# Kernel tuning notes

Measured on AMD Instinct MI355X. Metric: run time of the kernel, lower is better.

## Reference

```python
import jax, jax.numpy as jnp
import numpy as np

B, C, IMG, P = 8, 3, 64, 8
E, H, BS, L, NC = 256, 2, 8, 128, 10
HD = E // H
N = (IMG // P) ** 2 + 1  # 65 tokens (64 patches + cls)
NEG = -1e30  # stands in for -inf fill of block-diagonal scores
SCALE = float(np.sqrt(HD))


def _ln(x, g, b):
    m = jnp.mean(x, -1, keepdims=True)
    v = jnp.mean((x - m) ** 2, -1, keepdims=True)
    return (x - m) * jax.lax.rsqrt(v + 1e-5) * g + b


def _sparse_attn(x, wq, bq, wk, bk, wv, bv, fp):
    # Block-diagonal attention: only bs x bs diagonal blocks are finite, so we
    # reshape into non-overlapping blocks instead of materializing (B,N,H,N).
    Bx, Nx, Ex = x.shape
    q = (x @ wq + bq).reshape(Bx, Nx, H, HD)
    k = (x @ wk + bk).reshape(Bx, Nx, H, HD)
    v = (x @ wv + bv).reshape(Bx, Nx, H, HD)
    q = jnp.einsum('bnhe,ei->bnhi', q, fp)
    k = jnp.einsum('bnhe,ei->bnhi', k, fp)
    pad = (-Nx) % BS
    Np = Nx + pad
    G = Np // BS
    padf = lambda t: jnp.pad(t, ((0, 0), (0, pad), (0, 0), (0, 0)))
    qb = padf(q).reshape(Bx, G, BS, H, HD)
    kb = padf(k).reshape(Bx, G, BS, H, HD)
    vb = padf(v).reshape(Bx, G, BS, H, HD)
    scores = jnp.einsum('bgqhd,bgkhd->bgqhk', qb, kb) / SCALE  # (B,G,bs,H,bs)
    valid = (jnp.arange(Np) < Nx).reshape(G, BS)  # mask padded keys in last block
    scores = jnp.where(valid[None, :, None, None, :], scores, NEG)
    attn = jax.nn.softmax(scores, axis=-1)
    out = jnp.einsum('bgqhk,bgkhd->bgqhd', attn, vb).reshape(Bx, Np, Ex)
    return out[:, :Nx]


def setup_inputs() -> dict:
    key = jax.random.key(0)
    ks = jax.random.split(key, 12)
    s = 0.02
    f = lambda k, shp: (jax.random.normal(k, shp, jnp.float32) * s)
    z = lambda shp: jnp.zeros(shp, jnp.float32)
    o = lambda shp: jnp.ones(shp, jnp.float32)
    return {
        'src': jax.random.normal(ks[0], (B, C, IMG, IMG), jnp.float32),
        'conv_w': f(ks[1], (E, C, P, P)),
        'conv_b': z((E,)),
        'pos_emb': f(ks[2], (1, N, E)),
        'cls_tok': z((1, 1, E)),
        'Wq': f(ks[3], (L, E, E)), 'bq': z((L, E)),
        'Wk': f(ks[4], (L, E, E)), 'bk': z((L, E)),
        'Wv': f(ks[5], (L, E, E)), 'bv': z((L, E)),
        'fproj': f(ks[6], (L, HD, HD)),
        'ln1_g': o((L, E)), 'ln1_b': z((L, E)),
        'ln2_g': o((L, E)), 'ln2_b': z((L, E)),
        'ff1_w': f(ks[7], (L, E, 4 * E)), 'ff1_b': z((L, 4 * E)),
        'ff2_w': f(ks[8], (L, 4 * E, E)), 'ff2_b': z((L, E)),
        'fc_w': f(ks[9], (E, NC)), 'fc_b': z((NC,)),
    }


def reference(src, conv_w, conv_b, pos_emb, cls_tok, Wq, bq, Wk, bk, Wv, bv,
              fproj, ln1_g, ln1_b, ln2_g, ln2_b, ff1_w, ff1_b, ff2_w, ff2_b,
              fc_w, fc_b):
    # patch embedding (Conv2d stride=patch) -> flatten(2).transpose(1,2)
    x = jax.lax.conv_general_dilated(
        src, conv_w, (P, P), 'VALID',
        dimension_numbers=('NCHW', 'OIHW', 'NCHW')) + conv_b[None, :, None, None]
    x = x.reshape(B, E, -1).transpose(0, 2, 1)  # (B, num_patches, E)
    x = jnp.concatenate([jnp.broadcast_to(cls_tok, (B, 1, E)), x], axis=1)
    x = x + pos_emb

    params = (Wq, bq, Wk, bk, Wv, bv, fproj, ln1_g, ln1_b, ln2_g, ln2_b,
              ff1_w, ff1_b, ff2_w, ff2_b)

    def enc(h, p):
        wq, bq_, wk, bk_, wv, bv_, fp, g1, b1, g2, b2, w1, bb1, w2, bb2 = p
        h = h + _sparse_attn(_ln(h, g1, b1), wq, bq_, wk, bk_, wv, bv_, fp)
        hn = _ln(h, g2, b2)
        hf = jax.nn.gelu(hn @ w1 + bb1, approximate=False)  # dropout = eval identity
        h = h + hf @ w2 + bb2
        return h, None

    x, _ = jax.lax.scan(enc, x, params)
    return x[:, 0] @ fc_w + fc_b
```

## Files before the change

### kernel.cpp

```cpp
#include <hip/hip_runtime.h>
#include <math.h>

typedef __attribute__((ext_vector_type(8))) short short8v;
typedef __attribute__((ext_vector_type(4))) float float4v;

#if defined(__has_builtin)
#if __has_builtin(__builtin_amdgcn_global_load_lds)
#define USE_GLL 1
#endif
#endif
#ifndef USE_GLL
#define USE_GLL 0
#endif

__device__ __forceinline__ float gelu_f(float v) {
    return 0.5f * v * (1.0f + erff(v * 0.70710678118654752440f));
}

__device__ __forceinline__ unsigned short bf16r(float f) {
    unsigned u = __float_as_uint(f);
    u += 0x7FFFu + ((u >> 16) & 1u);
    return (unsigned short)(u >> 16);
}

__device__ __forceinline__ float bf2f(unsigned short s) {
    return __uint_as_float(((unsigned)s) << 16);
}

__global__ void dump_k(float* __restrict__ out, int n, float val) {
    int t = blockIdx.x * 256 + threadIdx.x;
    if (t < n) out[t] = val;
}

__global__ void tc_k(const float* __restrict__ in0, unsigned short* __restrict__ out0,
                     int R, int Cc, long long ils, long long ols) {
    __shared__ float tile[32][33];
    int l = blockIdx.z;
    const float* in = in0 + (size_t)l * ils;
    unsigned short* out = out0 + (size_t)l * ols;
    int t = threadIdx.x;
    int tx = t & 31, ty = t >> 5;
    int r0 = blockIdx.x * 32, c0 = blockIdx.y * 32;
#pragma unroll
    for (int i = 0; i < 4; ++i) {
        int r = r0 + ty + i * 8, c = c0 + tx;
        tile[ty + i * 8][tx] = (r < R && c < Cc) ? in[(size_t)r * Cc + c] : 0.f;
    }
    __syncthreads();
#pragma unroll
    for (int i = 0; i < 4; ++i) {
        int c = c0 + ty + i * 8, r = r0 + tx;
        if (c < Cc && r < R) out[(size_t)c * R + r] = bf16r(tile[tx][ty + i * 8]);
    }
}

__global__ void fold_k(const float* __restrict__ Wq0, const float* __restrict__ Wk0,
                       const float* __restrict__ fp0, unsigned short* __restrict__ Wt0,
                       int E, int HD, int mode) {
    extern __shared__ float fpS[];
    int l = blockIdx.z;
    long long EE = (long long)E * E;
    const float* fp = fp0 + (size_t)l * HD * HD;
    unsigned short* Wt = Wt0 + (size_t)l * 3 * EE;
    int t = threadIdx.x;
    int n0 = blockIdx.x * 64;
    int n = n0 + (t & 63);
    int cg = t >> 6;

    int i0 = 0;
    if (mode == 0) {
        for (int idx = t; idx < HD * HD; idx += 256) fpS[idx] = fp[idx];
    } else if (mode == 1) {
        int base = (n0 < E) ? n0 : n0 - E;
        i0 = base % HD;
        for (int idx = t; idx < HD * 64; idx += 256)
            fpS[idx] = fp[(size_t)(idx >> 6) * HD + i0 + (idx & 63)];
    }
    __syncthreads();
    if (n >= 2 * E) return;
    int s = (n >= E) ? 1 : 0;
    int idd = n - s * E;
    int h = idd / HD, i = idd % HD;
    const float* W = (s ? Wk0 : Wq0) + (size_t)l * EE;
    for (int c = cg; c < E; c += 4) {
        const float* Wr = W + (size_t)c * E + h * HD;
        float acc = 0.f;
        if (mode == 0) {
            for (int d = 0; d < HD; ++d) acc += Wr[d] * fpS[d * HD + i];
        } else if (mode == 1) {
            for (int d = 0; d < HD; ++d) acc += Wr[d] * fpS[d * 64 + (i - i0)];
        } else {
            for (int d = 0; d < HD; ++d) acc += Wr[d] * fp[(size_t)d * HD + i];
        }
        Wt[(size_t)n * E + c] = bf16r(acc);
    }
}

__global__ void biasfold_k(const float* __restrict__ bq0, const float* __restrict__ bk0,
                           const float* __restrict__ bv0, const float* __restrict__ fp0,
                           float* __restrict__ bqkv0, int E, int HD) {
    int l = blockIdx.z;
    const float* bq = bq0 + (size_t)l * E;
    const float* bk = bk0 + (size_t)l * E;
    const float* bv = bv0 + (size_t)l * E;
    const float* fp = fp0 + (size_t)l * HD * HD;
    float* bqkv = bqkv0 + (size_t)l * 3 * E;
    int c = blockIdx.x * 256 + threadIdx.x;
    if (c >= 3 * E) return;
    if (c < 2 * E) {
        int mat = c / E, cc = c % E, h = cc / HD, j = cc % HD;
        const float* bb = mat ? bk : bq;
        float s = 0.f;
        for (int d = 0; d < HD; ++d) s += bb[h * HD + d] * fp[(size_t)d * HD + j];
        bqkv[c] = s;
    } else {
        bqkv[c] = bv[c - 2 * E];
    }
}

__global__ __launch_bounds__(512) void gemm2_k(
        const unsigned short* __restrict__ A, int lda,
        const unsigned short* __restrict__ Bt, int ldbt,
        void* __restrict__ Cv, int ldc,
        const float* __restrict__ bias,
        int M, int Nn, int K, int op, int al, int nNt) {
    __shared__ unsigned short Ab[128 * 64];
    __shared__ unsigned short Bb[128 * 64];
    int t = threadIdx.x;
    int nwg = gridDim.x;
    int orig = blockIdx.x;
    int xcd = orig & 7, pos = orig >> 3;
    int q = nwg >> 3, r = nwg & 7;
    int wgid = (xcd < r ? xcd * (q + 1) : r * (q + 1) + (xcd - r) * q) + pos;
    int m0 = (wgid / nNt) * 128, n0 = (wgid % nNt) * 128;
    int w = t >> 6, lane = t & 63;
    int wm = w >> 2, wn = w & 3;
    int lrow = lane & 15, lk = lane >> 4;

    float4v acc[4][2];
#pragma unroll
    for (int fa = 0; fa < 4; ++fa)
#pragma unroll
        for (int fb = 0; fb < 2; ++fb) acc[fa][fb] = (float4v){0.f, 0.f, 0.f, 0.f};

    int srow8 = lane >> 3;
    int sch = lane & 7;
    bool fastA = al && (m0 + 128 <= M);
    bool fastB = al && (n0 + 128 <= Nn);

    for (int k0 = 0; k0 < K; k0 += 64) {
        bool fullK = (k0 + 64 <= K);
        __syncthreads();
#if USE_GLL
        if (fastA && fullK) {
#pragma unroll
            for (int it = 0; it < 2; ++it) {
                int rr = w * 16 + it * 8 + srow8;
                const unsigned short* g = A + (size_t)(m0 + rr) * lda + k0 + ((sch ^ (rr & 7)) << 3);
                __builtin_amdgcn_global_load_lds((const void*)g, (void*)&Ab[(w * 16 + it * 8) * 64], 16, 0, 0);
            }
        } else
#endif
        {
#pragma unroll
            for (int cc = 0; cc < 2; ++cc) {
                int c = t + cc * 512;
                int row = c >> 3, ch = c & 7;
                int gm = m0 + row, gk = k0 + ch * 8;
                short8v v = {0, 0, 0, 0, 0, 0, 0, 0};
                if (gm < M) {
                    if (al && gk + 8 <= K) {
                        v = *(const short8v*)(A + (size_t)gm * lda + gk);
                    } else {
                        const unsigned short* p = A + (size_t)gm * lda;
#pragma unroll
                        for (int j = 0; j < 8; ++j)
                            if (gk + j < K) v[j] = (short)p[gk + j];
                    }
                }
                *(short8v*)&Ab[row * 64 + ((ch ^ (row & 7)) << 3)] = v;
            }
        }
#if USE_GLL
        if (fastB && fullK) {
#pragma unroll
            for (int it = 0; it < 2; ++it) {
                int rr = w * 16 + it * 8 + srow8;
                const unsigned short* g = Bt + (size_t)(n0 + rr) * ldbt + k0 + ((sch ^ (rr & 7)) << 3);
                __builtin_amdgcn_global_load_lds((const void*)g, (void*)&Bb[(w * 16 + it * 8) * 64], 16, 0, 0);
            }
        } else
#endif
        {
#pragma unroll
            for (int cc = 0; cc < 2; ++cc) {
                int c = t + cc * 512;
                int row = c >> 3, ch = c & 7;
                int gn = n0 + row, gk = k0 + ch * 8;
                short8v v = {0, 0, 0, 0, 0, 0, 0, 0};
                if (gn < Nn) {
                    if (al && gk + 8 <= K) {
                        v = *(const short8v*)(Bt + (size_t)gn * ldbt + gk);
                    } else {
                        const unsigned short* p = Bt + (size_t)gn * ldbt;
#pragma unroll
                        for (int j = 0; j < 8; ++j)
                            if (gk + j < K) v[j] = (short)p[gk + j];
                    }
                }
                *(short8v*)&Bb[row * 64 + ((ch ^ (row & 7)) << 3)] = v;
            }
        }
        __syncthreads();
#pragma unroll
        for (int ks = 0; ks < 2; ++ks) {
            short8v af[4], bf[2];
#pragma unroll
            for (int fa = 0; fa < 4; ++fa) {
                int row = wm * 64 + fa * 16 + lrow;
                af[fa] = *(const short8v*)&Ab[row * 64 + (((ks * 4 + lk) ^ (row & 7)) << 3)];
            }
#pragma unroll
            for (int fb = 0; fb < 2; ++fb) {
                int row = wn * 32 + fb * 16 + lrow;
                bf[fb] = *(const short8v*)&Bb[row * 64 + (((ks * 4 + lk) ^ (row & 7)) << 3)];
            }
#pragma unroll
            for (int fa = 0; fa < 4; ++fa)
#pragma unroll
                for (int fb = 0; fb < 2; ++fb)
                    acc[fa][fb] = __builtin_amdgcn_mfma_f32_16x16x32_bf16(
                        af[fa], bf[fb], acc[fa][fb], 0, 0, 0);
        }
    }
    float* Cf = (float*)Cv;
    unsigned short* Cu = (unsigned short*)Cv;
#pragma unroll
    for (int fb = 0; fb < 2; ++fb) {
        int col = n0 + wn * 32 + fb * 16 + lrow;
        if (col >= Nn) continue;
        float bb = bias ? bias[col] : 0.f;
#pragma unroll
        for (int fa = 0; fa < 4; ++fa) {
#pragma unroll
            for (int q2 = 0; q2 < 4; ++q2) {
                int row = m0 + wm * 64 + fa * 16 + lk * 4 + q2;
                if (row >= M) continue;
                float v = acc[fa][fb][q2] + bb;
                size_t idx = (size_t)row * ldc + col;
                if (op == 0) Cf[idx] = v;
                else if (op == 1) Cu[idx] = bf16r(gelu_f(v));
                else if (op == 2) Cf[idx] += v;
                else Cu[idx] = bf16r(v);
            }
        }
    }
}

__global__ void embed_lds_k(const float* __restrict__ src, const float* __restrict__ cw,
                            const float* __restrict__ cb, const float* __restrict__ pos,
                            const float* __restrict__ cls, float* __restrict__ x,
                            int C, int IMG, int P, int m, int E, int N, int K) {
    extern __shared__ float patch[];
    int n = blockIdx.x, b = blockIdx.y, t = threadIdx.x;
    if (n == 0) {
        for (int e = t; e < E; e += 256)
            x[((size_t)b * N) * E + e] = cls[e] + pos[e];
        return;
    }
    int p = n - 1, ph = p / m, pw = p % m;
    int P2 = P * P;
    for (int mm = t; mm < K; mm += 256) {
        int c = mm / P2, rem = mm % P2, i = rem / P, j = rem % P;
        patch[mm] = src[(((size_t)b * C + c) * IMG + ph * P + i) * IMG + pw * P + j];
    }
    __syncthreads();
    for (int e = t; e < E; e += 256) {
        float acc = cb[e];
        const float* wr = cw + (size_t)e * K;
        for (int mm = 0; mm < K; ++mm) acc += patch[mm] * wr[mm];
        x[((size_t)b * N + n) * E + e] = acc + pos[(size_t)n * E + e];
    }
}

__global__ void embed_dir_k(const float* __restrict__ src, const float* __restrict__ cw,
                            const float* __restrict__ cb, const float* __restrict__ pos,
                            const float* __restrict__ cls, float* __restrict__ x,
                            int C, int IMG, int P, int m, int E, int N, int K) {
    int n = blockIdx.x, b = blockIdx.y, t = threadIdx.x;
    if (n == 0) {
        for (int e = t; e < E; e += 256)
            x[((size_t)b * N) * E + e] = cls[e] + pos[e];
        return;
    }
    int p = n - 1, ph = p / m, pw = p % m;
    int P2 = P * P;
    for (int e = t; e < E; e += 256) {
        float acc = cb[e];
        const float* wr = cw + (size_t)e * K;
        for (int mm = 0; mm < K; ++mm) {
            int c = mm / P2, rem = mm % P2, i = rem / P, j = rem % P;
            acc += src[(((size_t)b * C + c) * IMG + ph * P + i) * IMG + pw * P + j] * wr[mm];
        }
        x[((size_t)b * N + n) * E + e] = acc + pos[(size_t)n * E + e];
    }
}

__global__ void ln_k(const float* __restrict__ x, const float* __restrict__ g,
                     const float* __restrict__ b, unsigned short* __restrict__ xg,
                     int TOK, int E, float invE) {
    int row = blockIdx.x * 4 + (threadIdx.x >> 6);
    int lane = threadIdx.x & 63;
    if (row >= TOK) return;
    const float* xr = x + (size_t)row * E;
    float s = 0.f;
    for (int e = lane; e < E; e += 64) s += xr[e];
#pragma unroll
    for (int mm = 32; mm >= 1; mm >>= 1) s += __shfl_xor(s, mm, 64);
    float mean = s * invE;
    float v = 0.f;
    for (int e = lane; e < E; e += 64) { float d = xr[e] - mean; v += d * d; }
#pragma unroll
    for (int mm = 32; mm >= 1; mm >>= 1) v += __shfl_xor(v, mm, 64);
    float inv = rsqrtf(v * invE + 1e-5f);
    unsigned short* orow = xg + (size_t)row * E;
    for (int e = lane; e < E; e += 64)
        orow[e] = bf16r((xr[e] - mean) * inv * g[e] + b[e]);
}

__global__ void attn_sm_k(const unsigned short* __restrict__ qkv, float* __restrict__ x,
                          unsigned short* __restrict__ xg,
                          const float* __restrict__ g2, const float* __restrict__ b2,
                          int img0, int N, int E, int H, int HD, float rscale,
                          float invE, int vec) {
    extern __shared__ float sc[];
    int g = blockIdx.x, im = blockIdx.y, t = threadIdx.x;
    int t0 = g * 8, nv = min(8, N - t0);
    int E3 = 3 * E;
    const unsigned short* qb = qkv + ((size_t)im * N + t0) * E3;
    size_t rowbase = ((size_t)(img0 + im)) * N + t0;
    float* xb = x + rowbase * E;
    for (int idx = t; idx < H * 64; idx += 256) {
        int h = idx >> 6, qr = (idx >> 3) & 7, kr = idx & 7;
        float s = 0.f;
        if (qr < nv && kr < nv) {
            const unsigned short* qp = qb + (size_t)qr * E3 + h * HD;
            const unsigned short* kp = qb + (size_t)kr * E3 + E + h * HD;
            if (vec) {
                for (int d = 0; d < HD; d += 8) {
                    short8v qv = *(const short8v*)(qp + d);
                    short8v kv = *(const short8v*)(kp + d);
#pragma unroll
                    for (int j = 0; j < 8; ++j)
                        s += bf2f((unsigned short)qv[j]) * bf2f((unsigned short)kv[j]);
                }
            } else {
                for (int d = 0; d < HD; ++d)
                    s += bf2f(qp[d]) * bf2f(kp[d]);
            }
        }
        sc[idx] = s * rscale;
    }
    __syncthreads();
    for (int idx = t; idx < H * 8; idx += 256) {
        int h = idx >> 3, qr = idx & 7;
        if (qr < nv) {
            float* row = sc + h * 64 + qr * 8;
            float mx = -1e30f;
            for (int k = 0; k < nv; ++k) mx = fmaxf(mx, row[k]);
            float sum = 0.f;
            for (int k = 0; k < nv; ++k) { float e = expf(row[k] - mx); row[k] = e; sum += e; }
            float inv = 1.f / sum;
            for (int k = 0; k < nv; ++k) row[k] *= inv;
        }
    }
    __syncthreads();
    for (int c = t; c < E; c += 256) {
        int h = c / HD;
        const float* srow = sc + h * 64;
        float vcol[8];
#pragma unroll
        for (int k = 0; k < 8; ++k)
            vcol[k] = (k < nv) ? bf2f(qb[(size_t)k * E3 + 2 * E + c]) : 0.f;
        for (int r = 0; r < nv; ++r) {
            float o = 0.f;
#pragma unroll
            for (int k = 0; k < 8; ++k) o += srow[r * 8 + k] * vcol[k];
            xb[(size_t)r * E + c] += o;
        }
    }
    __syncthreads();
    int w = t >> 6, lane = t & 63;
#pragma unroll
    for (int rr = 0; rr < 2; ++rr) {
        int r = w + rr * 4;
        if (r >= nv) continue;
        const float* xr = xb + (size_t)r * E;
        float s = 0.f;
        for (int e = lane; e < E; e += 64) s += xr[e];
#pragma unroll
        for (int mm = 32; mm >= 1; mm >>= 1) s += __shfl_xor(s, mm, 64);
        float mean = s * invE;
        float v = 0.f;
        for (int e = lane; e < E; e += 64) { float d = xr[e] - mean; v += d * d; }
#pragma unroll
        for (int mm = 32; mm >= 1; mm >>= 1) v += __shfl_xor(v, mm, 64);
        float inv = rsqrtf(v * invE + 1e-5f);
        unsigned short* orow = xg + (rowbase + r) * E;
        for (int e = lane; e < E; e += 64)
            orow[e] = bf16r((xr[e] - mean) * inv * g2[e] + b2[e]);
    }
}

__global__ void head_k(const float* __restrict__ fw, const float* __restrict__ fb,
                       const float* __restrict__ x, float* __restrict__ out,
                       int Bc, int N, int E, int NC) {
    int idx = blockIdx.x * 256 + threadIdx.x;
    if (idx < Bc * NC) {
        int b = idx / NC, nc = idx % NC;
        float acc = fb[nc];
        const float* xr = x + (size_t)b * N * E;
        for (int e = 0; e < E; ++e) acc += xr[e] * fw[(size_t)e * NC + nc];
        out[idx] = acc;
    }
}

static int isqrt_i(long long v) {
    if (v < 0) return -1;
    long long r = (long long)(sqrt((double)v) + 0.5);
    while (r * r > v) --r;
    while ((r + 1) * (r + 1) <= v) ++r;
    return (int)r;
}

extern "C" void kernel_launch(void* const* d_in, const int* in_sizes, int n_in,
                              void* d_out, int out_size, void* d_ws, size_t ws_size,
                              hipStream_t stream) {
    float* out = (float*)d_out;
    int nblk_out = (out_size + 255) / 256;
#define DUMP(code, val) do { \
        dump_k<<<nblk_out, 256, 0, stream>>>(out, out_size, (float)((code) * 1000000.0 + (double)(val))); \
        return; } while (0)

    if (n_in != 22) DUMP(1, n_in < 999999 ? n_in : 999999);
    const int* S = in_sizes;

    int E = S[2];
    if (E <= 0 || S[4] != E) DUMP(2, 4);
    if (S[6] % E) DUMP(2, 6);
    int L = S[6] / E;
    if (L <= 0) DUMP(2, 6);
    long long EE = (long long)E * E;
    if (S[5] != L * EE || S[7] != L * EE || S[9] != L * EE) DUMP(2, 5);
    if (S[8] != L * E || S[10] != L * E) DUMP(2, 8);
    if (S[12] != L * E || S[13] != L * E || S[14] != L * E || S[15] != L * E) DUMP(2, 12);
    if (S[19] != L * E) DUMP(2, 19);
    if (S[11] % L) DUMP(2, 11);
    int HD = isqrt_i(S[11] / L);
    if ((long long)HD * HD * L != S[11] || HD <= 0 || E % HD) DUMP(3, HD > 0 ? HD : 0);
    int H = E / HD;
    if (S[17] % L) DUMP(2, 17);
    int FF = S[17] / L;
    if (S[16] != (long long)L * E * FF) DUMP(2, 16);
    if (S[18] != (long long)L * FF * E) DUMP(2, 18);
    if (S[3] % E) DUMP(2, 3);
    int N = S[3] / E;
    int m = isqrt_i(N - 1);
    if (m <= 0 || m * m != N - 1) DUMP(4, N < 999999 ? N : 999999);
    int NC = S[21];
    if (NC <= 0 || S[20] != (long long)E * NC) DUMP(2, 20);
    if (out_size % NC) DUMP(8, out_size < 999999 ? out_size : 999999);
    int Bc = out_size / NC;
    if (S[1] % E) DUMP(2, 1);
    int K = S[1] / E;
    static const int corder[12] = {3, 4, 1, 2, 8, 16, 6, 12, 32, 64, 24, 48};
    int C = -1, P = -1;
    for (int ci = 0; ci < 12; ++ci) {
        int c = corder[ci];
        if (K % c) continue;
        int p = isqrt_i(K / c);
        if (p > 0 && p * p * c == K) {
            long long img = (long long)p * m;
            if ((long long)Bc * c * img * img == S[0]) { C = c; P = p; break; }
        }
    }
    if (C < 0) DUMP(5, K < 999999 ? K : 999999);
    int IMG = P * m;
    int TOK = Bc * N;
    int Gg = (N + 7) / 8;
    int E3 = 3 * E;
    int al = ((E % 8) == 0 && (FF % 8) == 0) ? 1 : 0;
    int vecA = (al && (HD % 8) == 0) ? 1 : 0;

    int fmode;
    if (HD <= 64) fmode = 0;
    else if ((E % 64) == 0 && HD <= 256) fmode = 1;
    else fmode = 2;
    size_t fold_sh = (fmode == 0) ? (size_t)HD * HD * 4
                   : (fmode == 1) ? (size_t)HD * 64 * 4 : 16;

    size_t b_x  = ((size_t)TOK * E * 4 + 255) & ~(size_t)255;
    size_t b_xg = ((size_t)TOK * E * 2 + 255) & ~(size_t)255;
    size_t s_wt  = ((size_t)E3 * E * 2 + 255) & ~(size_t)255;
    size_t s_wff = ((size_t)E * FF * 2 + 255) & ~(size_t)255;
    size_t s_bq  = ((size_t)E3 * 4 + 255) & ~(size_t)255;
    size_t perL = s_wt + 2 * s_wff + s_bq;
    size_t minbuf = (size_t)N * E3 * 2;
    size_t fb2 = (size_t)128 * FF * 2;
    if (fb2 > minbuf) minbuf = fb2;

    int LW;
    if (b_x + b_xg + perL * L + minbuf <= ws_size) LW = L;
    else if (b_x + b_xg + perL + minbuf <= ws_size) LW = 1;
    else { DUMP(6, (double)(ws_size >> 20)); }

    char* wsb = (char*)d_ws;
    size_t off = 0;
    float* x = (float*)(wsb + off); off += b_x;
    unsigned short* xg = (unsigned short*)(wsb + off); off += b_xg;
    unsigned short* Wt_base = (unsigned short*)(wsb + off); off += s_wt * LW;
    unsigned short* w1t_base = (unsigned short*)(wsb + off); off += s_wff * LW;
    unsigned short* w2t_base = (unsigned short*)(wsb + off); off += s_wff * LW;
    float* bq_base = (float*)(wsb + off); off += s_bq * LW;
    size_t buf_bytes = ws_size - off;
    unsigned short* bufu = (unsigned short*)(wsb + off);

    int CHI = (int)(buf_bytes / ((size_t)N * E3 * 2));
    if (CHI > Bc) CHI = Bc;
    long long chf_l = (long long)(buf_bytes / ((size_t)FF * 2));
    chf_l = (chf_l / 128) * 128;
    int CHF = chf_l > TOK ? TOK : (int)chf_l;
    if (CHI < 1 || CHF < 128) DUMP(6, (double)(ws_size >> 20));

    const float* src = (const float*)d_in[0];
    const float* cw  = (const float*)d_in[1];
    const float* cb  = (const float*)d_in[2];
    const float* pos = (const float*)d_in[3];
    const float* cls = (const float*)d_in[4];
    const float* Wq  = (const float*)d_in[5];
    const float* bq  = (const float*)d_in[6];
    const float* Wk  = (const float*)d_in[7];
    const float* bk  = (const float*)d_in[8];
    const float* Wv  = (const float*)d_in[9];
    const float* bv  = (const float*)d_in[10];
    const float* fp  = (const float*)d_in[11];
    const float* g1  = (const float*)d_in[12];
    const float* b1  = (const float*)d_in[13];
    const float* g2  = (const float*)d_in[14];
    const float* b2  = (const float*)d_in[15];
    const float* w1  = (const float*)d_in[16];
    const float* bb1 = (const float*)d_in[17];
    const float* w2  = (const float*)d_in[18];
    const float* bb2 = (const float*)d_in[19];
    const float* fcw = (const float*)d_in[20];
    const float* fcb = (const float*)d_in[21];

    float invE = 1.f / (float)E;
    float rscale = 1.f / sqrtf((float)HD);
    size_t wtL = (size_t)E3 * E;
    size_t wffL = (size_t)E * FF;

    size_t patch_sh = (size_t)K * sizeof(float);
    if (patch_sh <= 48000)
        embed_lds_k<<<dim3(N, Bc), 256, patch_sh, stream>>>(src, cw, cb, pos, cls, x,
                                                            C, IMG, P, m, E, N, K);
    else
        embed_dir_k<<<dim3(N, Bc), 256, 0, stream>>>(src, cw, cb, pos, cls, x,
                                                     C, IMG, P, m, E, N, K);

    int gx_fold = (2 * E + 63) / 64;
    if (LW == L) {
        fold_k<<<dim3(gx_fold, 1, L), 256, fold_sh, stream>>>(Wq, Wk, fp, Wt_base, E, HD, fmode);
        tc_k<<<dim3((E + 31) / 32, (E + 31) / 32, L), 256, 0, stream>>>(
            Wv, Wt_base + (size_t)2 * E * E, E, E, EE, wtL);
        tc_k<<<dim3((E + 31) / 32, (FF + 31) / 32, L), 256, 0, stream>>>(
            w1, w1t_base, E, FF, (long long)E * FF, wffL);
        tc_k<<<dim3((FF + 31) / 32, (E + 31) / 32, L), 256, 0, stream>>>(
            w2, w2t_base, FF, E, (long long)E * FF, wffL);
        biasfold_k<<<dim3((E3 + 255) / 256, 1, L), 256, 0, stream>>>(
            bq, bk, bv, fp, bq_base, E, HD);
    }

    int ln_grid = (TOK + 3) / 4;
    size_t attn_sh = (size_t)H * 64 * sizeof(float);

    for (int l = 0; l < L; ++l) {
        int lw = (LW == L) ? l : 0;
        unsigned short* Wt_l  = Wt_base + (size_t)lw * (s_wt / 2);
        unsigned short* w1t_l = w1t_base + (size_t)lw * (s_wff / 2);
        unsigned short* w2t_l = w2t_base + (size_t)lw * (s_wff / 2);
        float* bq_l = (float*)((char*)bq_base + (size_t)lw * s_bq);

        if (LW != L) {
            fold_k<<<dim3(gx_fold, 1, 1), 256, fold_sh, stream>>>(
                Wq + (size_t)l * EE, Wk + (size_t)l * EE, fp + (size_t)l * HD * HD,
                Wt_l, E, HD, fmode);
            tc_k<<<dim3((E + 31) / 32, (E + 31) / 32, 1), 256, 0, stream>>>(
                Wv + (size_t)l * EE, Wt_l + (size_t)2 * E * E, E, E, 0, 0);
            tc_k<<<dim3((E + 31) / 32, (FF + 31) / 32, 1), 256, 0, stream>>>(
                w1 + (size_t)l * E * FF, w1t_l, E, FF, 0, 0);
            tc_k<<<dim3((FF + 31) / 32, (E + 31) / 32, 1), 256, 0, stream>>>(
                w2 + (size_t)l * FF * E, w2t_l, FF, E, 0, 0);
            biasfold_k<<<dim3((E3 + 255) / 256, 1, 1), 256, 0, stream>>>(
                bq + (size_t)l * E, bk + (size_t)l * E, bv + (size_t)l * E,
                fp + (size_t)l * HD * HD, bq_l, E, HD);
        }

        ln_k<<<ln_grid, 256, 0, stream>>>(x, g1 + (size_t)l * E, b1 + (size_t)l * E,
                                          xg, TOK, E, invE);
        for (int img0 = 0; img0 < Bc; img0 += CHI) {
            int nimg = Bc - img0 < CHI ? Bc - img0 : CHI;
            int ntok = nimg * N;
            int nMt = (ntok + 127) / 128, nNt = (E3 + 127) / 128;
            gemm2_k<<<nMt * nNt, 512, 0, stream>>>(
                xg + (size_t)img0 * N * E, E, Wt_l, E, bufu, E3, bq_l,
                ntok, E3, E, 3, al, nNt);
            attn_sm_k<<<dim3(Gg, nimg), 256, attn_sh, stream>>>(
                bufu, x, xg, g2 + (size_t)l * E, b2 + (size_t)l * E,
                img0, N, E, H, HD, rscale, invE, vecA);
        }
        for (int tok0 = 0; tok0 < TOK; tok0 += CHF) {
            int ntok = TOK - tok0 < CHF ? TOK - tok0 : CHF;
            int nMt = (ntok + 127) / 128;
            int nNt1 = (FF + 127) / 128, nNt2 = (E + 127) / 128;
            gemm2_k<<<nMt * nNt1, 512, 0, stream>>>(
                xg + (size_t)tok0 * E, E, w1t_l, E, bufu, FF,
                bb1 + (size_t)l * FF, ntok, FF, E, 1, al, nNt1);
            gemm2_k<<<nMt * nNt2, 512, 0, stream>>>(
                bufu, FF, w2t_l, FF, x + (size_t)tok0 * E, E,
                bb2 + (size_t)l * E, ntok, E, FF, 2, al, nNt2);
        }
    }
    head_k<<<nblk_out, 256, 0, stream>>>(fcw, fcb, x, out, Bc, N, E, NC);
#undef DUMP
}
```

Measured before the change: 10.15 ms.

## Add 256x256-tile pipelined bf16 MFMA GEMM with remainder fallback

Introduces a 256x256 tile GEMM kernel using direct global-to-LDS loads, XOR-swizzled LDS, double buffering, and XCD-aware block remapping, plus a launcher that splits M into a 256-aligned part and a remainder handled by the old 128-tile kernel. The FFN token chunk is rounded to multiples of 256. The intent is more data reuse per block and better overlap of loads with MFMA. At these small token counts it leaves very few blocks and adds an extra launch per GEMM.

```diff
diff --git a/kernel.cpp b/kernel.cpp
--- a/kernel.cpp
+++ b/kernel.cpp
@@ -254,6 +254,203 @@
                 else Cu[idx] = bf16r(v);
             }
         }
+    }
+}
+
+__global__ __launch_bounds__(512, 2) void gemm256_k(
+        const unsigned short* __restrict__ A, int lda,
+        const unsigned short* __restrict__ Bt, int ldbt,
+        void* __restrict__ Cv, int ldc,
+        const float* __restrict__ bias,
+        int M, int Nn, int K, int op, int nNt) {
+    extern __shared__ unsigned short lds[];
+    const int t = threadIdx.x;
+    const int w = t >> 6, lane = t & 63;
+    const int wm = w >> 2, wn = w & 3;
+    const int lrow = lane & 15, lk = lane >> 4;
+    int nwg = gridDim.x, orig = blockIdx.x;
+    int xcd = orig & 7, pos = orig >> 3;
+    int q = nwg >> 3, r = nwg & 7;
+    int wgid = (xcd < r ? xcd * (q + 1) : r * (q + 1) + (xcd - r) * q) + pos;
+    const int m0 = (wgid / nNt) * 256, n0 = (wgid % nNt) * 256;
+
+    const int sg_row = lane >> 3;
+    const int sg_ch = (lane & 7) ^ sg_row;
+
+    float4v acc[8][4];
+#pragma unroll
+    for (int fa = 0; fa < 8; ++fa)
+#pragma unroll
+        for (int fb = 0; fb < 4; ++fb) acc[fa][fb] = (float4v){0.f, 0.f, 0.f, 0.f};
+
+    const int nk = K >> 6;
+
+#if USE_GLL
+#define STAGE_A(KT, HALF, SLOT)                                                          \
+    {                                                                                    \
+        _Pragma("unroll")                                                                \
+        for (int it = 0; it < 2; ++it) {                                                 \
+            int rl = (HALF) * 128 + w * 16 + it * 8;                                     \
+            const unsigned short* g = A + (size_t)(m0 + rl + sg_row) * lda +             \
+                                      (KT) * 64 + (sg_ch << 3);                          \
+            __builtin_amdgcn_global_load_lds((const void*)g,                             \
+                (void*)&lds[(size_t)(SLOT) * 16384 + (size_t)rl * 64], 16, 0, 0);        \
+        }                                                                                \
+    }
+#define STAGE_B(KT, HALF, SLOT)                                                          \
+    {                                                                                    \
+        _Pragma("unroll")                                                                \
+        for (int it = 0; it < 2; ++it) {                                                 \
+            int rl = (HALF) * 128 + w * 16 + it * 8;                                     \
+            const unsigned short* g = Bt + (size_t)(n0 + rl + sg_row) * ldbt +           \
+                                      (KT) * 64 + (sg_ch << 3);                          \
+            __builtin_amdgcn_global_load_lds((const void*)g,                             \
+                (void*)&lds[32768 + (size_t)(SLOT) * 16384 + (size_t)rl * 64], 16, 0, 0);\
+        }                                                                                \
+    }
+#else
+#define STAGE_A(KT, HALF, SLOT)                                                          \
+    {                                                                                    \
+        _Pragma("unroll")                                                                \
+        for (int it = 0; it < 2; ++it) {                                                 \
+            int rl = (HALF) * 128 + w * 16 + it * 8;                                     \
+            const unsigned short* g = A + (size_t)(m0 + rl + sg_row) * lda +             \
+                                      (KT) * 64 + (sg_ch << 3);                          \
+            *(short8v*)&lds[(size_t)(SLOT) * 16384 + (size_t)(rl + sg_row) * 64 +        \
+                            ((size_t)((lane & 7)) << 3)] = *(const short8v*)g;           \
+        }                                                                                \
+    }
+#define STAGE_B(KT, HALF, SLOT)                                                          \
+    {                                                                                    \
+        _Pragma("unroll")                                                                \
+        for (int it = 0; it < 2; ++it) {                                                 \
+            int rl = (HALF) * 128 + w * 16 + it * 8;                                     \
+            const unsigned short* g = Bt + (size_t)(n0 + rl + sg_row) * ldbt +           \
+                                      (KT) * 64 + (sg_ch << 3);                          \
+            *(short8v*)&lds[32768 + (size_t)(SLOT) * 16384 + (size_t)(rl + sg_row) * 64 +\
+                            ((size_t)((lane & 7)) << 3)] = *(const short8v*)g;           \
+        }                                                                                \
+    }
+#endif
+
+    STAGE_A(0, 0, 0); STAGE_A(0, 1, 0); STAGE_B(0, 0, 0); STAGE_B(0, 1, 0);
+    if (nk > 1) { STAGE_B(1, 0, 1); STAGE_B(1, 1, 1); }
+    __builtin_amdgcn_sched_barrier(0);
+#if USE_GLL
+    if (nk > 1) asm volatile("s_waitcnt vmcnt(4)" ::: "memory");
+    else        asm volatile("s_waitcnt vmcnt(0)" ::: "memory");
+#else
+    asm volatile("s_waitcnt vmcnt(0)" ::: "memory");
+#endif
+    __builtin_amdgcn_sched_barrier(0);
+    __builtin_amdgcn_s_barrier();
+    __builtin_amdgcn_sched_barrier(0);
+
+    short8v breg[4][2];
+    for (int tt = 0; tt < nk; ++tt) {
+        const int s = tt & 1, sn = s ^ 1;
+        const bool doA = (tt + 1) < nk;
+        const bool doB = (tt + 2) < nk;
+        const size_t aBase = (size_t)s * 16384;
+        const size_t bBase = 32768 + (size_t)s * 16384;
+#pragma unroll
+        for (int p = 0; p < 4; ++p) {
+            short8v areg[2][2];
+            if (p == 0) {
+#pragma unroll
+                for (int fb = 0; fb < 4; ++fb) {
+                    int row = wn * 64 + fb * 16 + lrow;
+#pragma unroll
+                    for (int ks = 0; ks < 2; ++ks)
+                        breg[fb][ks] = *(const short8v*)&lds[bBase + (size_t)row * 64 +
+                            ((((ks << 2) + lk) ^ (row & 7)) << 3)];
+                }
+            }
+#pragma unroll
+            for (int i = 0; i < 2; ++i) {
+                int row = wm * 128 + (2 * p + i) * 16 + lrow;
+#pragma unroll
+                for (int ks = 0; ks < 2; ++ks)
+                    areg[i][ks] = *(const short8v*)&lds[aBase + (size_t)row * 64 +
+                        ((((ks << 2) + lk) ^ (row & 7)) << 3)];
+            }
+            if (p == 0 && doA) STAGE_A(tt + 1, 0, sn);
+            if (p == 1 && doA) STAGE_A(tt + 1, 1, sn);
+            if (p == 2 && doB) STAGE_B(tt + 2, 0, s);
+            if (p == 3 && doB) STAGE_B(tt + 2, 1, s);
+            __builtin_amdgcn_sched_barrier(0);
+            __builtin_amdgcn_s_barrier();
+            __builtin_amdgcn_sched_barrier(0);
+            __builtin_amdgcn_s_setprio(1);
+#pragma unroll
+            for (int i = 0; i < 2; ++i)
+#pragma unroll
+                for (int fb = 0; fb < 4; ++fb)
+#pragma unroll
+                    for (int ks = 0; ks < 2; ++ks)
+                        acc[2 * p + i][fb] = __builtin_amdgcn_mfma_f32_16x16x32_bf16(
+                            areg[i][ks], breg[fb][ks], acc[2 * p + i][fb], 0, 0, 0);
+            __builtin_amdgcn_s_setprio(0);
+            __builtin_amdgcn_sched_barrier(0);
+            if (p == 3) {
+#if USE_GLL
+                if (doB)      asm volatile("s_waitcnt vmcnt(4)" ::: "memory");
+                else if (doA) asm volatile("s_waitcnt vmcnt(0)" ::: "memory");
+#else
+                asm volatile("s_waitcnt vmcnt(0)" ::: "memory");
+#endif
+                __builtin_amdgcn_sched_barrier(0);
+            }
+            __builtin_amdgcn_s_barrier();
+            __builtin_amdgcn_sched_barrier(0);
+        }
+    }
+#undef STAGE_A
+#undef STAGE_B
+
+    float* Cf = (float*)Cv;
+    unsigned short* Cu = (unsigned short*)Cv;
+#pragma unroll
+    for (int fb = 0; fb < 4; ++fb) {
+        int col = n0 + wn * 64 + fb * 16 + lrow;
+        float bb = bias ? bias[col] : 0.f;
+#pragma unroll
+        for (int fa = 0; fa < 8; ++fa) {
+#pragma unroll
+            for (int q2 = 0; q2 < 4; ++q2) {
+                int row = m0 + wm * 128 + fa * 16 + lk * 4 + q2;
+                float v = acc[fa][fb][q2] + bb;
+                size_t idx = (size_t)row * ldc + col;
+                if (op == 0) Cf[idx] = v;
+                else if (op == 1) Cu[idx] = bf16r(gelu_f(v));
+                else if (op == 2) Cf[idx] += v;
+                else Cu[idx] = bf16r(v);
+            }
+        }
+    }
+}
+
+static inline void launch_gemm(const unsigned short* A, int lda,
+                               const unsigned short* Bt, int ldbt,
+                               void* Cv, int ldc, const float* bias,
+                               int M, int Nn, int K, int op, int al,
+                               hipStream_t stream) {
+    int M256 = 0;
+    if (al && Nn % 256 == 0 && K % 128 == 0 && K >= 128) M256 = (M / 256) * 256;
+    if (M256 > 0) {
+        int nNt = Nn / 256;
+        int grid = (M256 / 256) * nNt;
+        gemm256_k<<<grid, 512, 131072, stream>>>(A, lda, Bt, ldbt, Cv, ldc, bias,
+                                                 M256, Nn, K, op, nNt);
+    }
+    int Mr = M - M256;
+    if (Mr > 0) {
+        int esz = (op == 0 || op == 2) ? 4 : 2;
+        int nNt = (Nn + 127) / 128;
+        int grid = ((Mr + 127) / 128) * nNt;
+        gemm2_k<<<grid, 512, 0, stream>>>(A + (size_t)M256 * lda, lda, Bt, ldbt,
+                                          (void*)((char*)Cv + (size_t)M256 * ldc * esz),
+                                          ldc, bias, Mr, Nn, K, op, al, nNt);
     }
 }
 
@@ -492,6 +689,9 @@
     int al = ((E % 8) == 0 && (FF % 8) == 0) ? 1 : 0;
     int vecA = (al && (HD % 8) == 0) ? 1 : 0;
 
+    (void)hipFuncSetAttribute((const void*)gemm256_k,
+                              hipFuncAttributeMaxDynamicSharedMemorySize, 131072);
+
     int fmode;
     if (HD <= 64) fmode = 0;
     else if ((E % 64) == 0 && HD <= 256) fmode = 1;
@@ -528,7 +728,7 @@
     int CHI = (int)(buf_bytes / ((size_t)N * E3 * 2));
     if (CHI > Bc) CHI = Bc;
     long long chf_l = (long long)(buf_bytes / ((size_t)FF * 2));
-    chf_l = (chf_l / 128) * 128;
+    chf_l = (chf_l / 256) * 256;
     int CHF = chf_l > TOK ? TOK : (int)chf_l;
     if (CHI < 1 || CHF < 128) DUMP(6, (double)(ws_size >> 20));
 
@@ -611,24 +811,18 @@
         for (int img0 = 0; img0 < Bc; img0 += CHI) {
             int nimg = Bc - img0 < CHI ? Bc - img0 : CHI;
             int ntok = nimg * N;
-            int nMt = (ntok + 127) / 128, nNt = (E3 + 127) / 128;
-            gemm2_k<<<nMt * nNt, 512, 0, stream>>>(
-                xg + (size_t)img0 * N * E, E, Wt_l, E, bufu, E3, bq_l,
-                ntok, E3, E, 3, al, nNt);
+            launch_gemm(xg + (size_t)img0 * N * E, E, Wt_l, E, bufu, E3, bq_l,
+                        ntok, E3, E, 3, al, stream);
             attn_sm_k<<<dim3(Gg, nimg), 256, attn_sh, stream>>>(
                 bufu, x, xg, g2 + (size_t)l * E, b2 + (size_t)l * E,
                 img0, N, E, H, HD, rscale, invE, vecA);
         }
         for (int tok0 = 0; tok0 < TOK; tok0 += CHF) {
             int ntok = TOK - tok0 < CHF ? TOK - tok0 : CHF;
-            int nMt = (ntok + 127) / 128;
-            int nNt1 = (FF + 127) / 128, nNt2 = (E + 127) / 128;
-            gemm2_k<<<nMt * nNt1, 512, 0, stream>>>(
-                xg + (size_t)tok0 * E, E, w1t_l, E, bufu, FF,
-                bb1 + (size_t)l * FF, ntok, FF, E, 1, al, nNt1);
-            gemm2_k<<<nMt * nNt2, 512, 0, stream>>>(
-                bufu, FF, w2t_l, FF, x + (size_t)tok0 * E, E,
-                bb2 + (size_t)l * E, ntok, E, FF, 2, al, nNt2);
+            launch_gemm(xg + (size_t)tok0 * E, E, w1t_l, E, bufu, FF,
+                        bb1 + (size_t)l * FF, ntok, FF, E, 1, al, stream);
+            launch_gemm(bufu, FF, w2t_l, FF, x + (size_t)tok0 * E, E,
+                        bb2 + (size_t)l * E, ntok, E, FF, 2, al, stream);
         }
     }
     head_k<<<nblk_out, 256, 0, stream>>>(fcw, fcb, x, out, Bc, N, E, NC);
```

Result: slower. 23.33 ms (+129.8%).
